# Kernel optimization log

Measured on AMD Instinct MI355X. Metric: run time of the kernel, lower is better.

## Reference

```python
import jax, jax.numpy as jnp
import numpy as np

N_NODES = 100000
N_EDGES = 1600000
IN_CH = 128
HID = 32
HEADS = 4
OUT_CH = 32
NEG_SLOPE = 0.2  # PyG GATConv default


def setup_inputs() -> dict:
    key = jax.random.key(0)
    ks = jax.random.split(key, 12)
    s = 0.1
    x = jax.random.normal(ks[0], (N_NODES, IN_CH), dtype=jnp.float32)
    edge_index = jax.random.randint(ks[1], (2, N_EDGES), 0, N_NODES, dtype=jnp.int64)
    # layer 1: in -> heads*hid, concat
    W1 = jax.random.normal(ks[2], (IN_CH, HEADS * HID), dtype=jnp.float32) * s
    a_src1 = jax.random.normal(ks[3], (HEADS, HID), dtype=jnp.float32) * s
    a_dst1 = jax.random.normal(ks[4], (HEADS, HID), dtype=jnp.float32) * s
    b1 = jnp.zeros((HEADS * HID,), dtype=jnp.float32)
    # layer 2: heads*hid -> out, single head, averaged
    W2 = jax.random.normal(ks[5], (HEADS * HID, OUT_CH), dtype=jnp.float32) * s
    a_src2 = jax.random.normal(ks[6], (1, OUT_CH), dtype=jnp.float32) * s
    a_dst2 = jax.random.normal(ks[7], (1, OUT_CH), dtype=jnp.float32) * s
    b2 = jnp.zeros((OUT_CH,), dtype=jnp.float32)
    return {"x": x, "edge_index": edge_index, "W1": W1, "a_src1": a_src1,
            "a_dst1": a_dst1, "b1": b1, "W2": W2, "a_src2": a_src2,
            "a_dst2": a_dst2, "b2": b2}


def _gat_layer(x, src, dst, W, a_s, a_d, b, heads, ch, concat):
    n = x.shape[0]
    h = (x @ W).reshape(n, heads, ch)            # [N,H,C]
    alpha_s = jnp.einsum('nhc,hc->nh', h, a_s)   # [N,H]
    alpha_d = jnp.einsum('nhc,hc->nh', h, a_d)
    e = jax.nn.leaky_relu(alpha_s[src] + alpha_d[dst], NEG_SLOPE)  # [E,H]
    # segment softmax over edges sharing a destination (self-loops guarantee
    # every segment is non-empty)
    m = jax.ops.segment_max(e, dst, num_segments=n)
    ex = jnp.exp(e - m[dst])
    denom = jax.ops.segment_sum(ex, dst, num_segments=n)
    alpha = ex / (denom[dst] + 1e-16)            # [E,H]
    out = jax.ops.segment_sum(alpha[:, :, None] * h[src], dst, num_segments=n)  # [N,H,C]
    out = out.reshape(n, heads * ch) if concat else out.mean(axis=1)
    return out + b


def reference(x, edge_index, W1, a_src1, a_dst1, b1, W2, a_src2, a_dst2, b2):
    n = x.shape[0]
    loop = jnp.arange(n, dtype=edge_index.dtype)
    src = jnp.concatenate([edge_index[0], loop])  # add self-loops (PyG default)
    dst = jnp.concatenate([edge_index[1], loop])
    h = _gat_layer(x, src, dst, W1, a_src1, a_dst1, b1, HEADS, HID, True)
    h = jax.nn.relu(h)
    # dropout(p=0.5) is identity in eval mode
    out = _gat_layer(h, src, dst, W2, a_src2, a_dst2, b2, 1, OUT_CH, False)
    return out
```

## Files before the change

kernel.cpp:

```cpp
#include <hip/hip_runtime.h>
#include <math.h>

#define NEG_SLOPE 0.2f
#define EPB 8192

typedef __attribute__((ext_vector_type(8))) short bf16x8;
typedef __attribute__((ext_vector_type(4))) float f32x4;

__device__ __forceinline__ unsigned pack_bf16x2(float a, float b) {
    unsigned ua = __float_as_uint(a);
    unsigned ub = __float_as_uint(b);
    ua += 0x7FFFu + ((ua >> 16) & 1u);
    ub += 0x7FFFu + ((ub >> 16) & 1u);
    return (ua >> 16) | (ub & 0xFFFF0000u);
}
__device__ __forceinline__ unsigned short bf16r(float f) {
    unsigned u = __float_as_uint(f);
    u += 0x7FFFu + ((u >> 16) & 1u);
    return (unsigned short)(u >> 16);
}
__device__ __forceinline__ float bf_lo(unsigned u) { return __uint_as_float(u << 16); }
__device__ __forceinline__ float bf_hi(unsigned u) { return __uint_as_float(u & 0xFFFF0000u); }

#if defined(__has_builtin)
#if __has_builtin(__builtin_amdgcn_make_buffer_rsrc) && \
    __has_builtin(__builtin_amdgcn_raw_ptr_buffer_load_b32) && \
    __has_builtin(__builtin_amdgcn_raw_ptr_buffer_load_b64)
#define USE_BUFLD 1
#endif
#endif

#ifdef USE_BUFLD
typedef __amdgpu_buffer_rsrc_t Rsrc;
typedef __attribute__((ext_vector_type(2))) unsigned uint2v;
__device__ __forceinline__ Rsrc mkrsrc(const void* p) {
    return __builtin_amdgcn_make_buffer_rsrc((void*)p, (short)0, -1, 0x00020000);
}
__device__ __forceinline__ unsigned bufld_u32(Rsrc r, int voff) {
    return __builtin_amdgcn_raw_ptr_buffer_load_b32(r, voff, 0, 0);
}
__device__ __forceinline__ float bufld_f32(Rsrc r, int voff) {
    return __uint_as_float(__builtin_amdgcn_raw_ptr_buffer_load_b32(r, voff, 0, 0));
}
__device__ __forceinline__ uint2 bufld_u64(Rsrc r, int voff) {
    uint2v v = __builtin_amdgcn_raw_ptr_buffer_load_b64(r, voff, 0, 0);
    return make_uint2(v.x, v.y);
}
#else
struct Rsrc { const char* p; };
__device__ __forceinline__ Rsrc mkrsrc(const void* p) { Rsrc r; r.p = (const char*)p; return r; }
__device__ __forceinline__ unsigned bufld_u32(Rsrc r, int voff) { return *(const unsigned*)(r.p + voff); }
__device__ __forceinline__ float bufld_f32(Rsrc r, int voff) { return *(const float*)(r.p + voff); }
__device__ __forceinline__ uint2 bufld_u64(Rsrc r, int voff) { return *(const uint2*)(r.p + voff); }
#endif

#define SWZ(row, byteoff) ((((row) * 256) + (byteoff)) ^ (((row) & 15) << 4))


__global__ __launch_bounds__(256) void wcvt_kernel(const float* __restrict__ W1,
                                                   const float* __restrict__ W2,
                                                   unsigned short* __restrict__ W1T,
                                                   unsigned short* __restrict__ W2T) {
    int id = blockIdx.x * 256 + threadIdx.x;
    if (id < 16384) {
        int n = id >> 7, k = id & 127;
        W1T[id] = bf16r(W1[k * 128 + n]);
    } else if (id < 20480) {
        int j = id - 16384;
        int n = j >> 7, k = j & 127;
        W2T[j] = bf16r(W2[k * 32 + n]);
    }
}


__global__ __launch_bounds__(256) void gscan_bsum(const int* __restrict__ arr,
                                                  int* __restrict__ psum, int M) {
    __shared__ int red[4];
    int tid = threadIdx.x;
    int idx = blockIdx.x * 256 + tid;
    int v = (idx < M) ? arr[idx] : 0;
    #pragma unroll
    for (int off = 1; off < 64; off <<= 1) v += __shfl_xor(v, off, 64);
    if ((tid & 63) == 0) red[tid >> 6] = v;
    __syncthreads();
    if (tid == 0) psum[blockIdx.x] = red[0] + red[1] + red[2] + red[3];
}

__global__ __launch_bounds__(1024) void gscan_psum(int* __restrict__ psum, int nb) {
    __shared__ int ws[16];
    int tid = threadIdx.x, lane = tid & 63, w = tid >> 6;
    int v = (tid < nb) ? psum[tid] : 0;
    int incl = v;
    #pragma unroll
    for (int off = 1; off < 64; off <<= 1) {
        int t = __shfl_up(incl, off, 64);
        if (lane >= off) incl += t;
    }
    if (lane == 63) ws[w] = incl;
    __syncthreads();
    int wbase = 0;
    #pragma unroll
    for (int j = 0; j < 16; j++) { if (j < w) wbase += ws[j]; }
    if (tid < nb) psum[tid] = wbase + incl - v;
}

__global__ __launch_bounds__(256) void gscan_final(int* __restrict__ arr,
                                                   const int* __restrict__ psum, int M) {
    __shared__ int ws[4];
    int tid = threadIdx.x, lane = tid & 63, w = tid >> 6;
    int idx = blockIdx.x * 256 + tid;
    int v = (idx < M) ? arr[idx] : 0;
    int incl = v;
    #pragma unroll
    for (int off = 1; off < 64; off <<= 1) {
        int t = __shfl_up(incl, off, 64);
        if (lane >= off) incl += t;
    }
    if (lane == 63) ws[w] = incl;
    __syncthreads();
    int wbase = 0;
    #pragma unroll
    for (int j = 0; j < 4; j++) { if (j < w) wbase += ws[j]; }
    if (idx < M) arr[idx] = psum[blockIdx.x] + wbase + incl - v;
}


__global__ __launch_bounds__(256) void p1_hist(const int* __restrict__ dst, int E, int N,
                                               int nblk1, int nbuckets,
                                               int* __restrict__ partial) {
    __shared__ int hist[1024];
    int tid = threadIdx.x;
    for (int i = tid; i < nbuckets; i += 256) hist[i] = 0;
    __syncthreads();
    int base = blockIdx.x * EPB;
    int tot = E + N;
    #pragma unroll
    for (int it = 0; it < EPB / 256; it++) {
        int i = base + it * 256 + tid;
        if (i < tot) {
            int d = (i < E) ? dst[i] : (i - E);
            atomicAdd(&hist[d >> 8], 1);
        }
    }
    __syncthreads();
    for (int b = tid; b < nbuckets; b += 256)
        partial[b * nblk1 + blockIdx.x] = hist[b];
}

__global__ __launch_bounds__(256) void p1_scatter(const int* __restrict__ src,
                                                  const int* __restrict__ dst, int E, int N,
                                                  int nblk1, int nbuckets,
                                                  const int* __restrict__ scanned,
                                                  unsigned* __restrict__ pairs) {
    __shared__ int cursor[1024];
    int tid = threadIdx.x;
    for (int b = tid; b < nbuckets; b += 256)
        cursor[b] = scanned[b * nblk1 + blockIdx.x];
    __syncthreads();
    int base = blockIdx.x * EPB;
    int tot = E + N;
    #pragma unroll
    for (int it = 0; it < EPB / 256; it++) {
        int i = base + it * 256 + tid;
        if (i < tot) {
            int s = (i < E) ? src[i] : (i - E);
            int d = (i < E) ? dst[i] : (i - E);
            int pos = atomicAdd(&cursor[d >> 8], 1);
            pairs[pos] = ((unsigned)(d & 255) << 24) | (unsigned)s;
        }
    }
}

#define P2CAP 8192

__global__ __launch_bounds__(256) void p2_kernel(const unsigned* __restrict__ pairs,
                                                 const int* __restrict__ scanned,
                                                 int nblk1, int nbuckets, int Etot, int N,
                                                 int* __restrict__ rowptr,
                                                 int* __restrict__ col) {
    __shared__ unsigned buf[P2CAP];
    __shared__ int cnt[256];
    __shared__ int cur[256];
    __shared__ int wsum[4];
    int b = blockIdx.x;
    int tid = threadIdx.x, lane = tid & 63, w = tid >> 6;
    int bucketStart = scanned[b * nblk1];
    int bucketEnd = (b + 1 < nbuckets) ? scanned[(b + 1) * nblk1] : Etot;
    int sz = bucketEnd - bucketStart;
    bool inLds = (sz <= P2CAP);
    cnt[tid] = 0;
    if (inLds) {
        for (int i = tid; i < sz; i += 256) buf[i] = pairs[bucketStart + i];
    }
    __syncthreads();
    if (inLds) {
        for (int i = tid; i < sz; i += 256) atomicAdd(&cnt[buf[i] >> 24], 1);
    } else {
        for (int i = bucketStart + tid; i < bucketEnd; i += 256)
            atomicAdd(&cnt[pairs[i] >> 24], 1);
    }
    __syncthreads();
    int v = cnt[tid];
    int incl = v;
    #pragma unroll
    for (int off = 1; off < 64; off <<= 1) {
        int t = __shfl_up(incl, off, 64);
        if (lane >= off) incl += t;
    }
    if (lane == 63) wsum[w] = incl;
    __syncthreads();
    int wbase = 0;
    #pragma unroll
    for (int j = 0; j < 4; j++) { if (j < w) wbase += wsum[j]; }
    int base = bucketStart + wbase + incl - v;
    cur[tid] = base;
    int d = b * 256 + tid;
    if (d < N) rowptr[d] = base;
    if (b == nbuckets - 1 && tid == 0) rowptr[N] = Etot;
    __syncthreads();
    if (inLds) {
        for (int i = tid; i < sz; i += 256) {
            unsigned p = buf[i];
            int pos = atomicAdd(&cur[p >> 24], 1);
            col[pos] = (int)(p & 0xFFFFFFu);
        }
    } else {
        for (int i = bucketStart + tid; i < bucketEnd; i += 256) {
            unsigned p = pairs[i];
            int pos = atomicAdd(&cur[p >> 24], 1);
            col[pos] = (int)(p & 0xFFFFFFu);
        }
    }
}


__global__ __launch_bounds__(256) void gemm1_kernel(const float* __restrict__ x,
                                                    const unsigned short* __restrict__ W1T,
                                                    const float* __restrict__ a_s,
                                                    const float* __restrict__ a_d,
                                                    uint4* __restrict__ h1b,
                                                    float* __restrict__ as1,
                                                    float* __restrict__ ad1, int N) {
    __shared__ char xs[16384];
    __shared__ char wsm[32768];
    int tid = threadIdx.x;
    int row0 = blockIdx.x * 64;

    #pragma unroll
    for (int it = 0; it < 8; it++) {
        int idx = it * 256 + tid;
        int n = idx >> 4, kq = idx & 15;
        uint4 v = ((const uint4*)W1T)[idx];
        *(uint4*)(wsm + SWZ(n, kq * 16)) = v;
    }
    #pragma unroll
    for (int it = 0; it < 8; it++) {
        int idx = it * 256 + tid;
        int r = idx >> 5, k4 = idx & 31;
        int row = row0 + r;
        float4 v = (row < N) ? ((const float4*)x)[(size_t)row * 32 + k4]
                             : make_float4(0.f, 0.f, 0.f, 0.f);
        uint2 p;
        p.x = pack_bf16x2(v.x, v.y);
        p.y = pack_bf16x2(v.z, v.w);
        *(uint2*)(xs + SWZ(r, k4 * 8)) = p;
    }
    __syncthreads();

    int wv = tid >> 6, lane = tid & 63;
    int r0 = wv * 16;
    int lm = lane & 15, lk = lane >> 4;

    bf16x8 afr[4];
    #pragma unroll
    for (int ks = 0; ks < 4; ks++) {
        int row = r0 + lm;
        afr[ks] = *(const bf16x8*)(xs + SWZ(row, ks * 64 + lk * 16));
    }
    f32x4 acc[8];
    #pragma unroll
    for (int nt = 0; nt < 8; nt++) acc[nt] = (f32x4){0.f, 0.f, 0.f, 0.f};

    #pragma unroll
    for (int nt = 0; nt < 8; nt++) {
        int c = nt * 16 + lm;
        #pragma unroll
        for (int ks = 0; ks < 4; ks++) {
            bf16x8 bfr = *(const bf16x8*)(wsm + SWZ(c, ks * 64 + lk * 16));
            acc[nt] = __builtin_amdgcn_mfma_f32_16x16x32_bf16(afr[ks], bfr, acc[nt], 0, 0, 0);
        }
    }
    __syncthreads();

    #pragma unroll
    for (int nt = 0; nt < 8; nt++) {
        int c = nt * 16 + lm;
        #pragma unroll
        for (int e = 0; e < 4; e++) {
            int row = r0 + lk * 4 + e;
            *(unsigned short*)(xs + SWZ(row, c * 2)) = bf16r(acc[nt][e]);
        }
    }
    __syncthreads();

    #pragma unroll
    for (int it = 0; it < 4; it++) {
        int idx = it * 256 + tid;
        int row = idx >> 4, q = idx & 15;
        if (row0 + row < N) {
            uint4 v = *(const uint4*)(xs + SWZ(row, q * 16));
            h1b[(size_t)(row0 + row) * 16 + q] = v;
        }
    }
    {
        int row = tid >> 2, h = tid & 3;
        if (row0 + row < N) {
            float sd = 0.f, dd = 0.f;
            #pragma unroll
            for (int q = 0; q < 4; q++) {
                uint4 v = *(const uint4*)(xs + SWZ(row, h * 64 + q * 16));
                unsigned uu[4] = {v.x, v.y, v.z, v.w};
                #pragma unroll
                for (int j = 0; j < 4; j++) {
                    int k = h * 32 + q * 8 + 2 * j;
                    sd = fmaf(bf_lo(uu[j]), a_s[k], sd);
                    sd = fmaf(bf_hi(uu[j]), a_s[k + 1], sd);
                    dd = fmaf(bf_lo(uu[j]), a_d[k], dd);
                    dd = fmaf(bf_hi(uu[j]), a_d[k + 1], dd);
                }
            }
            as1[(row0 + row) * 4 + h] = sd;
            ad1[(row0 + row) * 4 + h] = dd;
        }
    }
}


__global__ __launch_bounds__(256) void agg1_kernel(const int* __restrict__ rowptr,
                                                   const int* __restrict__ col,
                                                   const unsigned* __restrict__ h1b,
                                                   const float* __restrict__ as1,
                                                   const float* __restrict__ ad1,
                                                   const float* __restrict__ b1,
                                                   unsigned* __restrict__ out1b, int N) {
    int lane = threadIdx.x & 63;
    int wid = __builtin_amdgcn_readfirstlane(threadIdx.x >> 6);
    int n = blockIdx.x * 4 + wid;
    if (n >= N) return;
    int hh = lane >> 4;
    float adn = ad1[n * 4 + hh];
    Rsrc h1r = mkrsrc(h1b);
    Rsrc asr = mkrsrc(as1);
    int laneByte = lane << 2;
    int hhByte = hh << 2;
    int exbase = lane & 48;
    int beg = __builtin_amdgcn_readfirstlane(rowptr[n]);
    int end = __builtin_amdgcn_readfirstlane(rowptr[n + 1]);
    float ax0 = 0.f, ay0 = 0.f, d0 = 0.f;
    float ax1 = 0.f, ay1 = 0.f, d1 = 0.f;
    float ax2 = 0.f, ay2 = 0.f, d2 = 0.f;
    float ax3 = 0.f, ay3 = 0.f, d3 = 0.f;
    int i = beg;
    for (; i + 16 <= end; i += 16) {
        int myss = col[i + (lane & 15)];
        float myl = bufld_f32(asr, (myss << 4) + hhByte);
        float e = myl + adn;
        e = fmaxf(e, e * NEG_SLOPE);
        float myex = __expf(e);
        int sj[16];
        #pragma unroll
        for (int j = 0; j < 16; j++) sj[j] = __shfl(myss, j, 64);
        unsigned uu[16];
        #pragma unroll
        for (int j = 0; j < 16; j++) uu[j] = bufld_u32(h1r, (sj[j] << 8) + laneByte);
        float exj[16];
        #pragma unroll
        for (int j = 0; j < 16; j++) exj[j] = __shfl(myex, exbase + j, 64);
        #pragma unroll
        for (int j = 0; j < 16; j++) {
            float ex = exj[j];
            if ((j & 3) == 0)      { d0 += ex; ax0 = fmaf(ex, bf_lo(uu[j]), ax0); ay0 = fmaf(ex, bf_hi(uu[j]), ay0); }
            else if ((j & 3) == 1) { d1 += ex; ax1 = fmaf(ex, bf_lo(uu[j]), ax1); ay1 = fmaf(ex, bf_hi(uu[j]), ay1); }
            else if ((j & 3) == 2) { d2 += ex; ax2 = fmaf(ex, bf_lo(uu[j]), ax2); ay2 = fmaf(ex, bf_hi(uu[j]), ay2); }
            else                   { d3 += ex; ax3 = fmaf(ex, bf_lo(uu[j]), ax3); ay3 = fmaf(ex, bf_hi(uu[j]), ay3); }
        }
    }
    for (; i + 4 <= end; i += 4) {
        int ss[4];
        unsigned uu[4];
        float ll[4];
        #pragma unroll
        for (int j = 0; j < 4; j++) ss[j] = col[i + j];
        #pragma unroll
        for (int j = 0; j < 4; j++) {
            uu[j] = bufld_u32(h1r, (ss[j] << 8) + laneByte);
            ll[j] = bufld_f32(asr, (ss[j] << 4) + hhByte);
        }
        #pragma unroll
        for (int j = 0; j < 4; j++) {
            float e = ll[j] + adn;
            e = fmaxf(e, e * NEG_SLOPE);
            float ex = __expf(e);
            if (j == 0)      { d0 += ex; ax0 = fmaf(ex, bf_lo(uu[j]), ax0); ay0 = fmaf(ex, bf_hi(uu[j]), ay0); }
            else if (j == 1) { d1 += ex; ax1 = fmaf(ex, bf_lo(uu[j]), ax1); ay1 = fmaf(ex, bf_hi(uu[j]), ay1); }
            else if (j == 2) { d2 += ex; ax2 = fmaf(ex, bf_lo(uu[j]), ax2); ay2 = fmaf(ex, bf_hi(uu[j]), ay2); }
            else             { d3 += ex; ax3 = fmaf(ex, bf_lo(uu[j]), ax3); ay3 = fmaf(ex, bf_hi(uu[j]), ay3); }
        }
    }
    for (; i < end; i++) {
        int s = col[i];
        unsigned u = bufld_u32(h1r, (s << 8) + laneByte);
        float l = bufld_f32(asr, (s << 4) + hhByte);
        float e = l + adn;
        e = fmaxf(e, e * NEG_SLOPE);
        float ex = __expf(e);
        d0 += ex;
        ax0 = fmaf(ex, bf_lo(u), ax0);
        ay0 = fmaf(ex, bf_hi(u), ay0);
    }
    float den = (d0 + d1) + (d2 + d3);
    float ax = (ax0 + ax1) + (ax2 + ax3);
    float ay = (ay0 + ay1) + (ay2 + ay3);
    float2 bb = ((const float2*)b1)[lane];
    float ox = fmaxf(ax / den + bb.x, 0.f);
    float oy = fmaxf(ay / den + bb.y, 0.f);
    out1b[n * 64 + lane] = pack_bf16x2(ox, oy);
}


__global__ __launch_bounds__(256) void gemm2_kernel(const uint4* __restrict__ out1b,
                                                    const unsigned short* __restrict__ W2T,
                                                    const float* __restrict__ a_s,
                                                    const float* __restrict__ a_d,
                                                    uint4* __restrict__ h2b,
                                                    float* __restrict__ as2,
                                                    float* __restrict__ ad2, int N) {
    __shared__ char xs[16384];
    __shared__ char wsm[8192];
    int tid = threadIdx.x;
    int row0 = blockIdx.x * 64;

    #pragma unroll
    for (int it = 0; it < 2; it++) {
        int idx = it * 256 + tid;
        int n = idx >> 4, kq = idx & 15;
        uint4 v = ((const uint4*)W2T)[idx];
        *(uint4*)(wsm + SWZ(n, kq * 16)) = v;
    }
    #pragma unroll
    for (int it = 0; it < 4; it++) {
        int idx = it * 256 + tid;
        int r = idx >> 4, q = idx & 15;
        int row = row0 + r;
        uint4 v = (row < N) ? out1b[(size_t)row * 16 + q] : make_uint4(0, 0, 0, 0);
        *(uint4*)(xs + SWZ(r, q * 16)) = v;
    }
    __syncthreads();

    int wv = tid >> 6, lane = tid & 63;
    int r0 = wv * 16;
    int lm = lane & 15, lk = lane >> 4;

    bf16x8 afr[4];
    #pragma unroll
    for (int ks = 0; ks < 4; ks++) {
        int row = r0 + lm;
        afr[ks] = *(const bf16x8*)(xs + SWZ(row, ks * 64 + lk * 16));
    }
    f32x4 acc[2];
    acc[0] = (f32x4){0.f, 0.f, 0.f, 0.f};
    acc[1] = (f32x4){0.f, 0.f, 0.f, 0.f};
    #pragma unroll
    for (int nt = 0; nt < 2; nt++) {
        int c = nt * 16 + lm;
        #pragma unroll
        for (int ks = 0; ks < 4; ks++) {
            bf16x8 bfr = *(const bf16x8*)(wsm + SWZ(c, ks * 64 + lk * 16));
            acc[nt] = __builtin_amdgcn_mfma_f32_16x16x32_bf16(afr[ks], bfr, acc[nt], 0, 0, 0);
        }
    }
    __syncthreads();

    #pragma unroll
    for (int nt = 0; nt < 2; nt++) {
        int c = nt * 16 + lm;
        #pragma unroll
        for (int e = 0; e < 4; e++) {
            int row = r0 + lk * 4 + e;
            *(unsigned short*)(xs + SWZ(row, c * 2)) = bf16r(acc[nt][e]);
        }
    }
    __syncthreads();

    {
        int row = tid >> 2, q = tid & 3;
        if (row0 + row < N) {
            uint4 v = *(const uint4*)(xs + SWZ(row, q * 16));
            h2b[(size_t)(row0 + row) * 4 + q] = v;
        }
    }
    if (tid < 64 && row0 + tid < N) {
        float sd = 0.f, dd = 0.f;
        #pragma unroll
        for (int q = 0; q < 4; q++) {
            uint4 v = *(const uint4*)(xs + SWZ(tid, q * 16));
            unsigned uu[4] = {v.x, v.y, v.z, v.w};
            #pragma unroll
            for (int j = 0; j < 4; j++) {
                int k = q * 8 + 2 * j;
                sd = fmaf(bf_lo(uu[j]), a_s[k], sd);
                sd = fmaf(bf_hi(uu[j]), a_s[k + 1], sd);
                dd = fmaf(bf_lo(uu[j]), a_d[k], dd);
                dd = fmaf(bf_hi(uu[j]), a_d[k + 1], dd);
            }
        }
        as2[row0 + tid] = sd;
        ad2[row0 + tid] = dd;
    }
}


#define A2SLOT(u, l)                                               \
    {                                                              \
        float e = l + adn;                                         \
        e = fmaxf(e, e * NEG_SLOPE);                               \
        float ex = __expf(e);                                      \
        den += ex;                                                 \
        a0 = fmaf(ex, bf_lo(u.x), a0);                             \
        a1 = fmaf(ex, bf_hi(u.x), a1);                             \
        a2 = fmaf(ex, bf_lo(u.y), a2);                             \
        a3 = fmaf(ex, bf_hi(u.y), a3);                             \
    }

__global__ __launch_bounds__(256) void agg2_kernel(const int* __restrict__ rowptr,
                                                   const int* __restrict__ col,
                                                   const unsigned* __restrict__ h2b,
                                                   const float* __restrict__ as2,
                                                   const float* __restrict__ ad2,
                                                   const float* __restrict__ b2,
                                                   float* __restrict__ out, int N) {
    int lane = threadIdx.x & 63;
    int wid = __builtin_amdgcn_readfirstlane(threadIdx.x >> 6);
    int n = blockIdx.x * 4 + wid;
    if (n >= N) return;
    int q8 = lane >> 3;
    int cl = lane & 7;
    Rsrc h2r = mkrsrc(h2b);
    Rsrc asr = mkrsrc(as2);
    int clByte = cl << 3;
    float adn = ad2[n];
    int beg = __builtin_amdgcn_readfirstlane(rowptr[n]);
    int end = __builtin_amdgcn_readfirstlane(rowptr[n + 1]);
    float a0 = 0.f, a1 = 0.f, a2 = 0.f, a3 = 0.f, den = 0.f;
    int i = beg;
    for (; i + 16 <= end; i += 16) {
        int e0 = i + q8, e1 = i + 8 + q8;
        int s0 = col[e0], s1 = col[e1];
        uint2 u0 = bufld_u64(h2r, (s0 << 6) + clByte);
        uint2 u1 = bufld_u64(h2r, (s1 << 6) + clByte);
        float l0 = bufld_f32(asr, s0 << 2);
        float l1 = bufld_f32(asr, s1 << 2);
        A2SLOT(u0, l0) A2SLOT(u1, l1)
    }
    for (; i < end; i += 8) {
        int e = i + q8;
        if (e < end) {
            int s = col[e];
            uint2 u = bufld_u64(h2r, (s << 6) + clByte);
            float l = bufld_f32(asr, s << 2);
            A2SLOT(u, l)
        }
    }
    den += __shfl_xor(den, 8, 64);
    den += __shfl_xor(den, 16, 64);
    den += __shfl_xor(den, 32, 64);
    a0 += __shfl_xor(a0, 8, 64);  a0 += __shfl_xor(a0, 16, 64);  a0 += __shfl_xor(a0, 32, 64);
    a1 += __shfl_xor(a1, 8, 64);  a1 += __shfl_xor(a1, 16, 64);  a1 += __shfl_xor(a1, 32, 64);
    a2 += __shfl_xor(a2, 8, 64);  a2 += __shfl_xor(a2, 16, 64);  a2 += __shfl_xor(a2, 32, 64);
    a3 += __shfl_xor(a3, 8, 64);  a3 += __shfl_xor(a3, 16, 64);  a3 += __shfl_xor(a3, 32, 64);
    if (q8 == 0) {
        float4 bb = ((const float4*)b2)[cl];
        float4 o;
        o.x = a0 / den + bb.x;
        o.y = a1 / den + bb.y;
        o.z = a2 / den + bb.z;
        o.w = a3 / den + bb.w;
        ((float4*)out)[n * 8 + cl] = o;
    }
}


extern "C" void kernel_launch(void* const* d_in, const int* in_sizes, int n_in,
                              void* d_out, int out_size, void* d_ws, size_t ws_size,
                              hipStream_t stream) {
    const float* x    = (const float*)d_in[0];
    const int*   ei   = (const int*)d_in[1];
    const float* W1   = (const float*)d_in[2];
    const float* a_s1 = (const float*)d_in[3];
    const float* a_d1 = (const float*)d_in[4];
    const float* b1   = (const float*)d_in[5];
    const float* W2   = (const float*)d_in[6];
    const float* a_s2 = (const float*)d_in[7];
    const float* a_d2 = (const float*)d_in[8];
    const float* b2   = (const float*)d_in[9];

    int N = in_sizes[0] / 128;
    int E = in_sizes[1] / 2;
    const int* srcA = ei;
    const int* dstA = ei + E;
    int Etot = E + N;

    char* ws = (char*)d_ws;
    size_t off = 0;
    auto alloc = [&](size_t bytes) {
        void* p = ws + off;
        off += (bytes + 255) & ~(size_t)255;
        return p;
    };
    unsigned* h1b   = (unsigned*)alloc((size_t)N * 128 * 2);
    unsigned* out1b = (unsigned*)alloc((size_t)N * 128 * 2);
    unsigned* h2b   = (unsigned*)alloc((size_t)N * 32 * 2);
    float* as1      = (float*)alloc((size_t)N * 4 * 4);
    float* ad1      = (float*)alloc((size_t)N * 4 * 4);
    float* as2      = (float*)alloc((size_t)N * 4);
    float* ad2      = (float*)alloc((size_t)N * 4);
    int*   rowptr   = (int*)alloc((size_t)(N + 1) * 4);
    int*   col      = (int*)alloc((size_t)Etot * 4);
    unsigned* pairs = (unsigned*)alloc((size_t)Etot * 4);
    unsigned short* W1T = (unsigned short*)alloc(128 * 128 * 2);
    unsigned short* W2T = (unsigned short*)alloc(32 * 128 * 2);

    int nbuckets = (N + 255) >> 8;
    int nblk1 = (Etot + EPB - 1) / EPB;
    int M = nbuckets * nblk1;
    int*   partial = (int*)alloc((size_t)M * 4);
    int nbs = (M + 255) / 256;
    int*   psum    = (int*)alloc((size_t)1024 * 4);

    hipLaunchKernelGGL(wcvt_kernel, dim3(80), dim3(256), 0, stream, W1, W2, W1T, W2T);
    hipLaunchKernelGGL(gemm1_kernel, dim3((N + 63) / 64), dim3(256), 0, stream,
                       x, W1T, a_s1, a_d1, (uint4*)h1b, as1, ad1, N);

    hipLaunchKernelGGL(p1_hist, dim3(nblk1), dim3(256), 0, stream,
                       dstA, E, N, nblk1, nbuckets, partial);
    hipLaunchKernelGGL(gscan_bsum, dim3(nbs), dim3(256), 0, stream, partial, psum, M);
    hipLaunchKernelGGL(gscan_psum, dim3(1), dim3(1024), 0, stream, psum, nbs);
    hipLaunchKernelGGL(gscan_final, dim3(nbs), dim3(256), 0, stream, partial, psum, M);
    hipLaunchKernelGGL(p1_scatter, dim3(nblk1), dim3(256), 0, stream,
                       srcA, dstA, E, N, nblk1, nbuckets, partial, pairs);
    hipLaunchKernelGGL(p2_kernel, dim3(nbuckets), dim3(256), 0, stream,
                       pairs, partial, nblk1, nbuckets, Etot, N, rowptr, col);

    hipLaunchKernelGGL(agg1_kernel, dim3((N + 3) / 4), dim3(256), 0, stream,
                       rowptr, col, h1b, as1, ad1, b1, out1b, N);
    hipLaunchKernelGGL(gemm2_kernel, dim3((N + 63) / 64), dim3(256), 0, stream,
                       (const uint4*)out1b, W2T, a_s2, a_d2, (uint4*)h2b, as2, ad2, N);
    hipLaunchKernelGGL(agg2_kernel, dim3((N + 3) / 4), dim3(256), 0, stream,
                       rowptr, col, h2b, as2, ad2, b2, (float*)d_out, N);
}
```

Before: 210.3 us.

## Merge weight conversion with histogram and CSR build with GEMM1 launches

Folds the weight-to-bf16 conversion into the histogram kernel and merges the CSR bucket-sort second pass with the first-layer GEMM into one launch, with blocks picking their role by block index. This cuts the number of launches and lets the independent GEMM work overlap with graph construction. The agg1 loop now reads column indices straight from memory and passes the row offset as the scalar offset of the buffer load, instead of broadcasting indices through shuffles. The merged kernel's LDS pool is sized for the GEMM role, which may lower occupancy for the CSR blocks, and a row offset that varies across lanes in the scalar slot may force extra readfirstlane loops.

```diff
diff --git a/kernel.cpp b/kernel.cpp
--- a/kernel.cpp
+++ b/kernel.cpp
@@ -39,6 +39,9 @@
 __device__ __forceinline__ unsigned bufld_u32(Rsrc r, int voff) {
     return __builtin_amdgcn_raw_ptr_buffer_load_b32(r, voff, 0, 0);
 }
+__device__ __forceinline__ unsigned bufld_u32s(Rsrc r, int voff, int soff) {
+    return __builtin_amdgcn_raw_ptr_buffer_load_b32(r, voff, soff, 0);
+}
 __device__ __forceinline__ float bufld_f32(Rsrc r, int voff) {
     return __uint_as_float(__builtin_amdgcn_raw_ptr_buffer_load_b32(r, voff, 0, 0));
 }
@@ -50,6 +53,7 @@
 struct Rsrc { const char* p; };
 __device__ __forceinline__ Rsrc mkrsrc(const void* p) { Rsrc r; r.p = (const char*)p; return r; }
 __device__ __forceinline__ unsigned bufld_u32(Rsrc r, int voff) { return *(const unsigned*)(r.p + voff); }
+__device__ __forceinline__ unsigned bufld_u32s(Rsrc r, int voff, int soff) { return *(const unsigned*)(r.p + voff + soff); }
 __device__ __forceinline__ float bufld_f32(Rsrc r, int voff) { return *(const float*)(r.p + voff); }
 __device__ __forceinline__ uint2 bufld_u64(Rsrc r, int voff) { return *(const uint2*)(r.p + voff); }
 #endif
@@ -57,19 +61,43 @@
 #define SWZ(row, byteoff) ((((row) * 256) + (byteoff)) ^ (((row) & 15) << 4))
 
 
-__global__ __launch_bounds__(256) void wcvt_kernel(const float* __restrict__ W1,
-                                                   const float* __restrict__ W2,
-                                                   unsigned short* __restrict__ W1T,
-                                                   unsigned short* __restrict__ W2T) {
-    int id = blockIdx.x * 256 + threadIdx.x;
-    if (id < 16384) {
-        int n = id >> 7, k = id & 127;
-        W1T[id] = bf16r(W1[k * 128 + n]);
-    } else if (id < 20480) {
-        int j = id - 16384;
-        int n = j >> 7, k = j & 127;
-        W2T[j] = bf16r(W2[k * 32 + n]);
-    }
+__global__ __launch_bounds__(256) void wcvt_hist_kernel(const float* __restrict__ W1,
+                                                        const float* __restrict__ W2,
+                                                        unsigned short* __restrict__ W1T,
+                                                        unsigned short* __restrict__ W2T,
+                                                        const int* __restrict__ dst,
+                                                        int E, int N, int nblk1, int nbuckets,
+                                                        int* __restrict__ partial) {
+    if (blockIdx.x < 80) {
+        int id = blockIdx.x * 256 + threadIdx.x;
+        if (id < 16384) {
+            int n = id >> 7, k = id & 127;
+            W1T[id] = bf16r(W1[k * 128 + n]);
+        } else if (id < 20480) {
+            int j = id - 16384;
+            int n = j >> 7, k = j & 127;
+            W2T[j] = bf16r(W2[k * 32 + n]);
+        }
+        return;
+    }
+    int blk = blockIdx.x - 80;
+    __shared__ int hist[1024];
+    int tid = threadIdx.x;
+    for (int i = tid; i < nbuckets; i += 256) hist[i] = 0;
+    __syncthreads();
+    int base = blk * EPB;
+    int tot = E + N;
+    #pragma unroll
+    for (int it = 0; it < EPB / 256; it++) {
+        int i = base + it * 256 + tid;
+        if (i < tot) {
+            int d = (i < E) ? dst[i] : (i - E);
+            atomicAdd(&hist[d >> 8], 1);
+        }
+    }
+    __syncthreads();
+    for (int b = tid; b < nbuckets; b += 256)
+        partial[b * nblk1 + blk] = hist[b];
 }
 
 
@@ -124,28 +152,6 @@
     if (idx < M) arr[idx] = psum[blockIdx.x] + wbase + incl - v;
 }
 
-
-__global__ __launch_bounds__(256) void p1_hist(const int* __restrict__ dst, int E, int N,
-                                               int nblk1, int nbuckets,
-                                               int* __restrict__ partial) {
-    __shared__ int hist[1024];
-    int tid = threadIdx.x;
-    for (int i = tid; i < nbuckets; i += 256) hist[i] = 0;
-    __syncthreads();
-    int base = blockIdx.x * EPB;
-    int tot = E + N;
-    #pragma unroll
-    for (int it = 0; it < EPB / 256; it++) {
-        int i = base + it * 256 + tid;
-        if (i < tot) {
-            int d = (i < E) ? dst[i] : (i - E);
-            atomicAdd(&hist[d >> 8], 1);
-        }
-    }
-    __syncthreads();
-    for (int b = tid; b < nbuckets; b += 256)
-        partial[b * nblk1 + blockIdx.x] = hist[b];
-}
 
 __global__ __launch_bounds__(256) void p1_scatter(const int* __restrict__ src,
                                                   const int* __restrict__ dst, int E, int N,
@@ -173,78 +179,77 @@
 
 #define P2CAP 8192
 
-__global__ __launch_bounds__(256) void p2_kernel(const unsigned* __restrict__ pairs,
-                                                 const int* __restrict__ scanned,
-                                                 int nblk1, int nbuckets, int Etot, int N,
-                                                 int* __restrict__ rowptr,
-                                                 int* __restrict__ col) {
-    __shared__ unsigned buf[P2CAP];
-    __shared__ int cnt[256];
-    __shared__ int cur[256];
-    __shared__ int wsum[4];
-    int b = blockIdx.x;
-    int tid = threadIdx.x, lane = tid & 63, w = tid >> 6;
-    int bucketStart = scanned[b * nblk1];
-    int bucketEnd = (b + 1 < nbuckets) ? scanned[(b + 1) * nblk1] : Etot;
-    int sz = bucketEnd - bucketStart;
-    bool inLds = (sz <= P2CAP);
-    cnt[tid] = 0;
-    if (inLds) {
-        for (int i = tid; i < sz; i += 256) buf[i] = pairs[bucketStart + i];
-    }
-    __syncthreads();
-    if (inLds) {
-        for (int i = tid; i < sz; i += 256) atomicAdd(&cnt[buf[i] >> 24], 1);
-    } else {
-        for (int i = bucketStart + tid; i < bucketEnd; i += 256)
-            atomicAdd(&cnt[pairs[i] >> 24], 1);
-    }
-    __syncthreads();
-    int v = cnt[tid];
-    int incl = v;
-    #pragma unroll
-    for (int off = 1; off < 64; off <<= 1) {
-        int t = __shfl_up(incl, off, 64);
-        if (lane >= off) incl += t;
-    }
-    if (lane == 63) wsum[w] = incl;
-    __syncthreads();
-    int wbase = 0;
-    #pragma unroll
-    for (int j = 0; j < 4; j++) { if (j < w) wbase += wsum[j]; }
-    int base = bucketStart + wbase + incl - v;
-    cur[tid] = base;
-    int d = b * 256 + tid;
-    if (d < N) rowptr[d] = base;
-    if (b == nbuckets - 1 && tid == 0) rowptr[N] = Etot;
-    __syncthreads();
-    if (inLds) {
-        for (int i = tid; i < sz; i += 256) {
-            unsigned p = buf[i];
-            int pos = atomicAdd(&cur[p >> 24], 1);
-            col[pos] = (int)(p & 0xFFFFFFu);
-        }
-    } else {
-        for (int i = bucketStart + tid; i < bucketEnd; i += 256) {
-            unsigned p = pairs[i];
-            int pos = atomicAdd(&cur[p >> 24], 1);
-            col[pos] = (int)(p & 0xFFFFFFu);
-        }
-    }
-}
-
-
-__global__ __launch_bounds__(256) void gemm1_kernel(const float* __restrict__ x,
-                                                    const unsigned short* __restrict__ W1T,
-                                                    const float* __restrict__ a_s,
-                                                    const float* __restrict__ a_d,
-                                                    uint4* __restrict__ h1b,
-                                                    float* __restrict__ as1,
-                                                    float* __restrict__ ad1, int N) {
-    __shared__ char xs[16384];
-    __shared__ char wsm[32768];
+
+__global__ __launch_bounds__(256) void p2_gemm1_kernel(
+        const unsigned* __restrict__ pairs, const int* __restrict__ scanned,
+        int nblk1, int nbuckets, int Etot, int N,
+        int* __restrict__ rowptr, int* __restrict__ col,
+        const float* __restrict__ x, const unsigned short* __restrict__ W1T,
+        const float* __restrict__ a_s, const float* __restrict__ a_d,
+        uint4* __restrict__ h1b, float* __restrict__ as1, float* __restrict__ ad1) {
+    __shared__ char pool[49152];
     int tid = threadIdx.x;
-    int row0 = blockIdx.x * 64;
+
+    if ((int)blockIdx.x < nbuckets) {
+        unsigned* buf = (unsigned*)pool;
+        int* cnt = (int*)(pool + 32768);
+        int* cur = (int*)(pool + 33792);
+        int* wsum = (int*)(pool + 34816);
+        int b = blockIdx.x;
+        int lane = tid & 63, w = tid >> 6;
+        int bucketStart = scanned[b * nblk1];
+        int bucketEnd = (b + 1 < nbuckets) ? scanned[(b + 1) * nblk1] : Etot;
+        int sz = bucketEnd - bucketStart;
+        bool inLds = (sz <= P2CAP);
+        cnt[tid] = 0;
+        if (inLds) {
+            for (int i = tid; i < sz; i += 256) buf[i] = pairs[bucketStart + i];
+        }
+        __syncthreads();
+        if (inLds) {
+            for (int i = tid; i < sz; i += 256) atomicAdd(&cnt[buf[i] >> 24], 1);
+        } else {
+            for (int i = bucketStart + tid; i < bucketEnd; i += 256)
+                atomicAdd(&cnt[pairs[i] >> 24], 1);
+        }
+        __syncthreads();
+        int v = cnt[tid];
+        int incl = v;
+        #pragma unroll
+        for (int off = 1; off < 64; off <<= 1) {
+            int t = __shfl_up(incl, off, 64);
+            if (lane >= off) incl += t;
+        }
+        if (lane == 63) wsum[w] = incl;
+        __syncthreads();
+        int wbase = 0;
+        #pragma unroll
+        for (int j = 0; j < 4; j++) { if (j < w) wbase += wsum[j]; }
+        int base = bucketStart + wbase + incl - v;
+        cur[tid] = base;
+        int d = b * 256 + tid;
+        if (d < N) rowptr[d] = base;
+        if (b == nbuckets - 1 && tid == 0) rowptr[N] = Etot;
+        __syncthreads();
+        if (inLds) {
+            for (int i = tid; i < sz; i += 256) {
+                unsigned p = buf[i];
+                int pos = atomicAdd(&cur[p >> 24], 1);
+                col[pos] = (int)(p & 0xFFFFFFu);
+            }
+        } else {
+            for (int i = bucketStart + tid; i < bucketEnd; i += 256) {
+                unsigned p = pairs[i];
+                int pos = atomicAdd(&cur[p >> 24], 1);
+                col[pos] = (int)(p & 0xFFFFFFu);
+            }
+        }
+        return;
+    }
+
+    char* xs = pool;
+    char* wsm = pool + 16384;
+    int row0 = ((int)blockIdx.x - nbuckets) * 64;
 
     #pragma unroll
     for (int it = 0; it < 8; it++) {
@@ -367,12 +372,12 @@
         float e = myl + adn;
         e = fmaxf(e, e * NEG_SLOPE);
         float myex = __expf(e);
-        int sj[16];
-        #pragma unroll
-        for (int j = 0; j < 16; j++) sj[j] = __shfl(myss, j, 64);
         unsigned uu[16];
         #pragma unroll
-        for (int j = 0; j < 16; j++) uu[j] = bufld_u32(h1r, (sj[j] << 8) + laneByte);
+        for (int j = 0; j < 16; j++) {
+            int sj = col[i + j];
+            uu[j] = bufld_u32s(h1r, laneByte, sj << 8);
+        }
         float exj[16];
         #pragma unroll
         for (int j = 0; j < 16; j++) exj[j] = __shfl(myex, exbase + j, 64);
@@ -386,15 +391,13 @@
         }
     }
     for (; i + 4 <= end; i += 4) {
-        int ss[4];
         unsigned uu[4];
         float ll[4];
         #pragma unroll
-        for (int j = 0; j < 4; j++) ss[j] = col[i + j];
-        #pragma unroll
         for (int j = 0; j < 4; j++) {
-            uu[j] = bufld_u32(h1r, (ss[j] << 8) + laneByte);
-            ll[j] = bufld_f32(asr, (ss[j] << 4) + hhByte);
+            int sj = col[i + j];
+            uu[j] = bufld_u32s(h1r, laneByte, sj << 8);
+            ll[j] = bufld_f32(asr, (sj << 4) + hhByte);
         }
         #pragma unroll
         for (int j = 0; j < 4; j++) {
@@ -409,7 +412,7 @@
     }
     for (; i < end; i++) {
         int s = col[i];
-        unsigned u = bufld_u32(h1r, (s << 8) + laneByte);
+        unsigned u = bufld_u32s(h1r, laneByte, s << 8);
         float l = bufld_f32(asr, (s << 4) + hhByte);
         float e = l + adn;
         e = fmaxf(e, e * NEG_SLOPE);
@@ -637,23 +640,22 @@
     int nbs = (M + 255) / 256;
     int*   psum    = (int*)alloc((size_t)1024 * 4);
 
-    hipLaunchKernelGGL(wcvt_kernel, dim3(80), dim3(256), 0, stream, W1, W2, W1T, W2T);
-    hipLaunchKernelGGL(gemm1_kernel, dim3((N + 63) / 64), dim3(256), 0, stream,
-                       x, W1T, a_s1, a_d1, (uint4*)h1b, as1, ad1, N);
-
-    hipLaunchKernelGGL(p1_hist, dim3(nblk1), dim3(256), 0, stream,
-                       dstA, E, N, nblk1, nbuckets, partial);
+    int gblocks = (N + 63) / 64;
+
+    hipLaunchKernelGGL(wcvt_hist_kernel, dim3(80 + nblk1), dim3(256), 0, stream,
+                       W1, W2, W1T, W2T, dstA, E, N, nblk1, nbuckets, partial);
     hipLaunchKernelGGL(gscan_bsum, dim3(nbs), dim3(256), 0, stream, partial, psum, M);
     hipLaunchKernelGGL(gscan_psum, dim3(1), dim3(1024), 0, stream, psum, nbs);
     hipLaunchKernelGGL(gscan_final, dim3(nbs), dim3(256), 0, stream, partial, psum, M);
     hipLaunchKernelGGL(p1_scatter, dim3(nblk1), dim3(256), 0, stream,
                        srcA, dstA, E, N, nblk1, nbuckets, partial, pairs);
-    hipLaunchKernelGGL(p2_kernel, dim3(nbuckets), dim3(256), 0, stream,
-                       pairs, partial, nblk1, nbuckets, Etot, N, rowptr, col);
+    hipLaunchKernelGGL(p2_gemm1_kernel, dim3(nbuckets + gblocks), dim3(256), 0, stream,
+                       pairs, partial, nblk1, nbuckets, Etot, N, rowptr, col,
+                       x, W1T, a_s1, a_d1, (uint4*)h1b, as1, ad1);
 
     hipLaunchKernelGGL(agg1_kernel, dim3((N + 3) / 4), dim3(256), 0, stream,
                        rowptr, col, h1b, as1, ad1, b1, out1b, N);
-    hipLaunchKernelGGL(gemm2_kernel, dim3((N + 63) / 64), dim3(256), 0, stream,
+    hipLaunchKernelGGL(gemm2_kernel, dim3(gblocks), dim3(256), 0, stream,
                        (const uint4*)out1b, W2T, a_s2, a_d2, (uint4*)h2b, as2, ad2, N);
     hipLaunchKernelGGL(agg2_kernel, dim3((N + 3) / 4), dim3(256), 0, stream,
                        rowptr, col, h2b, as2, ad2, b2, (float*)d_out, N);
```

After: 194.6 us, median of 2. -7.4%, faster.
